# Optimization experiments

Hardware: AMD Instinct MI355X
Metric: run time of the kernel (lower is better)

Reference implementation:

```python
import jax, jax.numpy as jnp
import numpy as np


def setup_inputs() -> dict:
    key = jax.random.key(0)
    ks = jax.random.split(key, 4)
    B, T, D, U = 64, 2048, 128, 128
    enc = jax.random.normal(ks[0], (B, T, D), dtype=jnp.float32)
    # Keras Dense default: glorot_uniform kernel, zero bias; use scaled normals here.
    W1_w = jax.random.normal(ks[1], (D, U), dtype=jnp.float32) / np.sqrt(D)
    W2_w = jax.random.normal(ks[2], (D, U), dtype=jnp.float32) / np.sqrt(D)
    V_w = jax.random.normal(ks[3], (U, 1), dtype=jnp.float32) / np.sqrt(U)
    return {
        "encoder_outputs": enc,
        "W1_w": W1_w,
        "W1_b": jnp.zeros((U,), jnp.float32),
        "W2_w": W2_w,
        "W2_b": jnp.zeros((U,), jnp.float32),
        "V_w": V_w,
        "V_b": jnp.zeros((1,), jnp.float32),
    }


def reference(encoder_outputs, W1_w, W1_b, W2_w, W2_b, V_w, V_b):
    # score = V(tanh(W1(x) + W2(x)))  -> [B, T, 1]
    # W1(x)+W2(x) == x @ (W1_w + W2_w) + (W1_b + W2_b); keep faithful but fused.
    h = jnp.tanh(jnp.einsum("btd,du->btu", encoder_outputs, W1_w) + W1_b
                 + jnp.einsum("btd,du->btu", encoder_outputs, W2_w) + W2_b)
    score = jnp.einsum("btu,uo->bto", h, V_w) + V_b  # [B, T, 1]
    attn = jax.nn.softmax(score, axis=1)             # softmax over sequence axis
    # context = sum_t attn[b,t,0] * x[b,t,:]
    context = jnp.einsum("bto,btd->bd", attn, encoder_outputs)
    return context
```

## Files before the change

### kernel.cpp

```cpp
#include <hip/hip_runtime.h>
#include <hip/hip_bf16.h>

#define DD 128
#define UU 128
#define SEQ_T 2048
#define ROWS 64
#define NCHUNK 32

typedef __attribute__((ext_vector_type(8))) short short8;
typedef __attribute__((ext_vector_type(4))) float f32x4;

__device__ __forceinline__ unsigned short f2bf(float f) {
  unsigned u = __float_as_uint(f);
  u += 0x7fffu + ((u >> 16) & 1u);
  return (unsigned short)(u >> 16);
}
__device__ __forceinline__ float bf2f(unsigned short s) {
  return __uint_as_float(((unsigned)s) << 16);
}
__device__ __forceinline__ float fast_tanh(float v) {
  float z = __expf(2.0f * v);
  return 1.0f - __fdividef(2.0f, z + 1.0f);
}

#define WT_OFF   0
#define BIAS_OFF 33280
#define MW_OFF   33792
#define LW_OFF   41984
#define EW_OFF   50176

__global__ void prep_kernel(const float* __restrict__ W1w, const float* __restrict__ W1b,
                            const float* __restrict__ W2w, const float* __restrict__ W2b,
                            unsigned short* __restrict__ wt_g, float* __restrict__ bias_g,
                            float* __restrict__ out)
{
  int i = blockIdx.x * 256 + threadIdx.x;
  int u = i >> 7, d = i & 127;
  float s = W1w[(size_t)d * UU + u] + W2w[(size_t)d * UU + u];
  wt_g[(size_t)u * DD + d] = f2bf(s);
  if (i < UU) bias_g[i] = W1b[i] + W2b[i];
  if (threadIdx.x < 128) out[(size_t)blockIdx.x * DD + threadIdx.x] = 0.0f;
}

__global__ __launch_bounds__(256, 4)
void scores_kernel(const float* __restrict__ x,
                   const unsigned short* __restrict__ wt_g,
                   const float* __restrict__ bias_g,
                   const float* __restrict__ Vw,
                   float* __restrict__ mw, float* __restrict__ lw,
                   float* __restrict__ e_ws)
{
  __shared__ __align__(16) unsigned short xs[ROWS * DD];
  __shared__ __align__(16) float spart[4][ROWS];

  const int tid = threadIdx.x;
  const int blk = blockIdx.x;
  const int rowbase = blk * ROWS;
  const int w = tid >> 6, l = tid & 63, lx = l & 15, lq = l >> 4;

  float4 xr[8];
  #pragma unroll
  for (int it = 0; it < 4; ++it) {
    int F = tid + 256 * it;
    int row = F >> 4, g = F & 15;
    const float* src = x + (size_t)(rowbase + row) * DD + g * 8;
    xr[2 * it]     = *reinterpret_cast<const float4*>(src);
    xr[2 * it + 1] = *reinterpret_cast<const float4*>(src + 4);
  }

  short8 Bf[2][4];
  float vs[2], bs[2];
  #pragma unroll
  for (int nf = 0; nf < 2; ++nf) {
    const int u = 32 * w + 16 * nf + lx;
    vs[nf] = Vw[u];
    bs[nf] = bias_g[u];
    #pragma unroll
    for (int kf = 0; kf < 4; ++kf)
      Bf[nf][kf] = *reinterpret_cast<const short8*>(
          wt_g + (size_t)u * DD + 32 * kf + 8 * lq);
  }

  #pragma unroll
  for (int it = 0; it < 4; ++it) {
    int F = tid + 256 * it;
    int row = F >> 4, g = F & 15;
    float4 v0 = xr[2 * it], v1 = xr[2 * it + 1];
    short8 pk;
    pk[0] = (short)f2bf(v0.x); pk[1] = (short)f2bf(v0.y);
    pk[2] = (short)f2bf(v0.z); pk[3] = (short)f2bf(v0.w);
    pk[4] = (short)f2bf(v1.x); pk[5] = (short)f2bf(v1.y);
    pk[6] = (short)f2bf(v1.z); pk[7] = (short)f2bf(v1.w);
    *reinterpret_cast<short8*>(xs + row * DD + ((g ^ (row & 15)) << 3)) = pk;
  }
  __syncthreads();

  f32x4 acc[4][2];
  #pragma unroll
  for (int mf = 0; mf < 4; ++mf) {
    acc[mf][0] = (f32x4){0.f, 0.f, 0.f, 0.f};
    acc[mf][1] = (f32x4){0.f, 0.f, 0.f, 0.f};
  }
  #pragma unroll
  for (int kf = 0; kf < 4; ++kf) {
    const int gs8 = ((4 * kf + lq) ^ lx) << 3;
    #pragma unroll
    for (int mf = 0; mf < 4; ++mf) {
      short8 a = *reinterpret_cast<const short8*>(xs + (16 * mf + lx) * DD + gs8);
      acc[mf][0] = __builtin_amdgcn_mfma_f32_16x16x32_bf16(a, Bf[0][kf], acc[mf][0], 0, 0, 0);
      acc[mf][1] = __builtin_amdgcn_mfma_f32_16x16x32_bf16(a, Bf[1][kf], acc[mf][1], 0, 0, 0);
    }
  }

  #pragma unroll
  for (int mf = 0; mf < 4; ++mf) {
    #pragma unroll
    for (int r = 0; r < 4; ++r) {
      float p = vs[0] * fast_tanh(acc[mf][0][r] + bs[0])
              + vs[1] * fast_tanh(acc[mf][1][r] + bs[1]);
      p += __shfl_xor(p, 1);
      p += __shfl_xor(p, 2);
      p += __shfl_xor(p, 4);
      p += __shfl_xor(p, 8);
      if (lx == 0) spart[w][16 * mf + 4 * lq + r] = p;
    }
  }
  __syncthreads();

  float sv = (spart[0][l] + spart[1][l]) + (spart[2][l] + spart[3][l]);
  float m = sv;
  #pragma unroll
  for (int off = 1; off < 64; off <<= 1) m = fmaxf(m, __shfl_xor(m, off));
  float e = __expf(sv - m);
  float lsum = e;
  #pragma unroll
  for (int off = 1; off < 64; off <<= 1) lsum += __shfl_xor(lsum, off);

  if (w == 0) e_ws[(size_t)blk * ROWS + l] = e;
  if (tid == 0) { mw[blk] = m; lw[blk] = lsum; }
}

__global__ __launch_bounds__(256, 8)
void context_kernel(const float* __restrict__ x,
                    const float* __restrict__ mw, const float* __restrict__ lw,
                    const float* __restrict__ e_ws,
                    float* __restrict__ out)
{
  __shared__ __align__(16) float pctx[4][DD];

  const int tid = threadIdx.x;
  const int blk = blockIdx.x;
  const int rowbase = blk * ROWS;
  const int b = blk >> 5;
  const int c = blk & 31;
  const int w = tid >> 6, l = tid & 63;
  const int gd = tid & 15;
  const int tg = tid >> 4;

  float mi = mw[b * NCHUNK + (l & 31)];
  float li = lw[b * NCHUNK + (l & 31)];
  float M = mi;
  #pragma unroll
  for (int off = 1; off < 32; off <<= 1) M = fmaxf(M, __shfl_xor(M, off));
  float term = __expf(mi - M) * li;
  float L = term;
  #pragma unroll
  for (int off = 1; off < 32; off <<= 1) L += __shfl_xor(L, off);
  const float mc = __shfl(mi, c & 31);
  const float alpha = __fdividef(__expf(mc - M), L);

  float ca[8];
  #pragma unroll
  for (int e2 = 0; e2 < 8; ++e2) ca[e2] = 0.0f;
  #pragma unroll
  for (int k = 0; k < 4; ++k) {
    const int row = tg * 4 + k;
    const float wgt = alpha * e_ws[(size_t)blk * ROWS + row];
    const float* src = x + (size_t)(rowbase + row) * DD + gd * 8;
    const float4 v0 = *reinterpret_cast<const float4*>(src);
    const float4 v1 = *reinterpret_cast<const float4*>(src + 4);
    ca[0] = fmaf(wgt, v0.x, ca[0]); ca[1] = fmaf(wgt, v0.y, ca[1]);
    ca[2] = fmaf(wgt, v0.z, ca[2]); ca[3] = fmaf(wgt, v0.w, ca[3]);
    ca[4] = fmaf(wgt, v1.x, ca[4]); ca[5] = fmaf(wgt, v1.y, ca[5]);
    ca[6] = fmaf(wgt, v1.z, ca[6]); ca[7] = fmaf(wgt, v1.w, ca[7]);
  }
  #pragma unroll
  for (int e2 = 0; e2 < 8; ++e2) {
    ca[e2] += __shfl_xor(ca[e2], 16);
    ca[e2] += __shfl_xor(ca[e2], 32);
  }
  if (l < 16) {
    #pragma unroll
    for (int e2 = 0; e2 < 8; ++e2) pctx[w][l * 8 + e2] = ca[e2];
  }
  __syncthreads();

  if (tid < 128) {
    float c0 = (pctx[0][tid] + pctx[1][tid]) + (pctx[2][tid] + pctx[3][tid]);
    atomicAdd(&out[(size_t)b * DD + tid], c0);
  }
}

extern "C" void kernel_launch(void* const* d_in, const int* in_sizes, int n_in,
                              void* d_out, int out_size, void* d_ws, size_t ws_size,
                              hipStream_t stream)
{
  const float* x   = (const float*)d_in[0];
  const float* W1w = (const float*)d_in[1];
  const float* W1b = (const float*)d_in[2];
  const float* W2w = (const float*)d_in[3];
  const float* W2b = (const float*)d_in[4];
  const float* Vw  = (const float*)d_in[5];

  const int bt = in_sizes[0] / DD;
  const int nblk = bt / ROWS;

  char* ws = (char*)d_ws;
  unsigned short* wt_g = (unsigned short*)(ws + WT_OFF);
  float* bias_g = (float*)(ws + BIAS_OFF);
  float* mw   = (float*)(ws + MW_OFF);
  float* lw   = (float*)(ws + LW_OFF);
  float* e_ws = (float*)(ws + EW_OFF);
  float* out  = (float*)d_out;

  prep_kernel<<<64, 256, 0, stream>>>(W1w, W1b, W2w, W2b, wt_g, bias_g, out);
  scores_kernel<<<nblk, 256, 0, stream>>>(x, wt_g, bias_g, Vw, mw, lw, e_ws);
  context_kernel<<<nblk, 256, 0, stream>>>(x, mw, lw, e_ws, out);
}
```

Baseline: 39.25 us.

## Stage weight matrix in LDS and swap MFMA operands so each wave owns rows

The scores kernel now copies the full bf16 weight matrix into swizzled shared memory and transposes the MFMA roles. Weights become the A operand and x rows the B operand, so each wave handles 16 rows across all 128 units. That lets the V-weighted tanh reduction finish with two cross-lane shuffles instead of a 16-lane shuffle tree per output. The cost is 32KB more LDS per block, occupancy lowered to 3 blocks, and extra LDS reads of weights per wave. The bf16 conversion also switches to the library intrinsic, and the bias offset moves.

Measured after the change: 38.31 us. 1.02x faster.

```diff
diff --git a/kernel.cpp b/kernel.cpp
--- a/kernel.cpp
+++ b/kernel.cpp
@@ -11,9 +11,7 @@
 typedef __attribute__((ext_vector_type(4))) float f32x4;
 
 __device__ __forceinline__ unsigned short f2bf(float f) {
-  unsigned u = __float_as_uint(f);
-  u += 0x7fffu + ((u >> 16) & 1u);
-  return (unsigned short)(u >> 16);
+  return __builtin_bit_cast(unsigned short, __float2bfloat16(f));
 }
 __device__ __forceinline__ float bf2f(unsigned short s) {
   return __uint_as_float(((unsigned)s) << 16);
@@ -24,7 +22,7 @@
 }
 
 #define WT_OFF   0
-#define BIAS_OFF 33280
+#define BIAS_OFF 32768
 #define MW_OFF   33792
 #define LW_OFF   41984
 #define EW_OFF   50176
@@ -42,7 +40,7 @@
   if (threadIdx.x < 128) out[(size_t)blockIdx.x * DD + threadIdx.x] = 0.0f;
 }
 
-__global__ __launch_bounds__(256, 4)
+__global__ __launch_bounds__(256, 3)
 void scores_kernel(const float* __restrict__ x,
                    const unsigned short* __restrict__ wt_g,
                    const float* __restrict__ bias_g,
@@ -51,7 +49,10 @@
                    float* __restrict__ e_ws)
 {
   __shared__ __align__(16) unsigned short xs[ROWS * DD];
-  __shared__ __align__(16) float spart[4][ROWS];
+  __shared__ __align__(16) unsigned short wtl[UU * DD];
+  __shared__ __align__(16) float bsum[UU];
+  __shared__ __align__(16) float vv[UU];
+  __shared__ float slds[ROWS];
 
   const int tid = threadIdx.x;
   const int blk = blockIdx.x;
@@ -68,18 +69,14 @@
     xr[2 * it + 1] = *reinterpret_cast<const float4*>(src + 4);
   }
 
-  short8 Bf[2][4];
-  float vs[2], bs[2];
-  #pragma unroll
-  for (int nf = 0; nf < 2; ++nf) {
-    const int u = 32 * w + 16 * nf + lx;
-    vs[nf] = Vw[u];
-    bs[nf] = bias_g[u];
-    #pragma unroll
-    for (int kf = 0; kf < 4; ++kf)
-      Bf[nf][kf] = *reinterpret_cast<const short8*>(
-          wt_g + (size_t)u * DD + 32 * kf + 8 * lq);
-  }
+  #pragma unroll
+  for (int it = 0; it < 8; ++it) {
+    int F = tid + 256 * it;
+    int u = F >> 4, g = F & 15;
+    short8 wv = *reinterpret_cast<const short8*>(wt_g + (size_t)F * 8);
+    *reinterpret_cast<short8*>(wtl + u * DD + ((g ^ (u & 15)) << 3)) = wv;
+  }
+  if (tid < UU) { bsum[tid] = bias_g[tid]; vv[tid] = Vw[tid]; }
 
   #pragma unroll
   for (int it = 0; it < 4; ++it) {
@@ -95,39 +92,35 @@
   }
   __syncthreads();
 
-  f32x4 acc[4][2];
-  #pragma unroll
-  for (int mf = 0; mf < 4; ++mf) {
-    acc[mf][0] = (f32x4){0.f, 0.f, 0.f, 0.f};
-    acc[mf][1] = (f32x4){0.f, 0.f, 0.f, 0.f};
-  }
+  f32x4 acc[8];
+  #pragma unroll
+  for (int nf = 0; nf < 8; ++nf) acc[nf] = (f32x4){0.f, 0.f, 0.f, 0.f};
   #pragma unroll
   for (int kf = 0; kf < 4; ++kf) {
     const int gs8 = ((4 * kf + lq) ^ lx) << 3;
+    short8 bx = *reinterpret_cast<const short8*>(xs + (16 * w + lx) * DD + gs8);
     #pragma unroll
-    for (int mf = 0; mf < 4; ++mf) {
-      short8 a = *reinterpret_cast<const short8*>(xs + (16 * mf + lx) * DD + gs8);
-      acc[mf][0] = __builtin_amdgcn_mfma_f32_16x16x32_bf16(a, Bf[0][kf], acc[mf][0], 0, 0, 0);
-      acc[mf][1] = __builtin_amdgcn_mfma_f32_16x16x32_bf16(a, Bf[1][kf], acc[mf][1], 0, 0, 0);
+    for (int nf = 0; nf < 8; ++nf) {
+      short8 aw = *reinterpret_cast<const short8*>(wtl + (16 * nf + lx) * DD + gs8);
+      acc[nf] = __builtin_amdgcn_mfma_f32_16x16x32_bf16(aw, bx, acc[nf], 0, 0, 0);
     }
   }
 
-  #pragma unroll
-  for (int mf = 0; mf < 4; ++mf) {
+  float p = 0.0f;
+  #pragma unroll
+  for (int nf = 0; nf < 8; ++nf) {
+    const f32x4 bs4 = *reinterpret_cast<const f32x4*>(bsum + 16 * nf + 4 * lq);
+    const f32x4 vs4 = *reinterpret_cast<const f32x4*>(vv + 16 * nf + 4 * lq);
     #pragma unroll
-    for (int r = 0; r < 4; ++r) {
-      float p = vs[0] * fast_tanh(acc[mf][0][r] + bs[0])
-              + vs[1] * fast_tanh(acc[mf][1][r] + bs[1]);
-      p += __shfl_xor(p, 1);
-      p += __shfl_xor(p, 2);
-      p += __shfl_xor(p, 4);
-      p += __shfl_xor(p, 8);
-      if (lx == 0) spart[w][16 * mf + 4 * lq + r] = p;
-    }
-  }
+    for (int r = 0; r < 4; ++r)
+      p += vs4[r] * fast_tanh(acc[nf][r] + bs4[r]);
+  }
+  p += __shfl_xor(p, 16);
+  p += __shfl_xor(p, 32);
+  if (l < 16) slds[16 * w + l] = p;
   __syncthreads();
 
-  float sv = (spart[0][l] + spart[1][l]) + (spart[2][l] + spart[3][l]);
+  float sv = slds[l];
   float m = sv;
   #pragma unroll
   for (int off = 1; off < 64; off <<= 1) m = fmaxf(m, __shfl_xor(m, off));
```
